# Kernel tuning notes

Hardware: AMD Instinct MI355X
Metric: run time of the kernel (lower is better)

## Reference

```python
import jax, jax.numpy as jnp
import numpy as np

B, S, D = 2, 1024, 4096          # batch, prefill seqlen, model dim
H, KVH, HD = 32, 8, 128          # q heads, kv heads, head dim
MAX = 2048                       # kv-cache capacity
THETA = 1000000.0
REP = H // KVH


def _rope_tables(pos):
    # pos: [S] int -> cos/sin [S, HD]
    inv_freq = 1.0 / (THETA ** (jnp.arange(0, HD, 2, dtype=jnp.float32) / HD))
    freqs = pos[:, None].astype(jnp.float32) * inv_freq[None, :]
    emb = jnp.concatenate([freqs, freqs], axis=-1)
    return jnp.cos(emb), jnp.sin(emb)


def _rotate_half(t):
    t1, t2 = jnp.split(t, 2, axis=-1)
    return jnp.concatenate([-t2, t1], axis=-1)


def setup_inputs() -> dict:
    key = jax.random.key(0)
    k = jax.random.split(key, 8)
    sc = 1.0 / np.sqrt(D)
    x = jax.random.normal(k[0], (B, S, D), jnp.float32)
    storage_idx = jnp.arange(S, dtype=jnp.int32)
    cache = jnp.zeros((2, 1, B, KVH, MAX, HD), jnp.float32)
    causal = jnp.tril(jnp.ones((MAX, MAX), bool))
    mask = jnp.where(causal, 0.0, -1e9).astype(jnp.float32)
    Wq = jax.random.normal(k[1], (D, H * HD), jnp.float32) * sc
    bq = jax.random.normal(k[2], (H * HD,), jnp.float32) * 0.01
    Wk = jax.random.normal(k[3], (D, KVH * HD), jnp.float32) * sc
    bk = jax.random.normal(k[4], (KVH * HD,), jnp.float32) * 0.01
    Wv = jax.random.normal(k[5], (D, KVH * HD), jnp.float32) * sc
    bv = jax.random.normal(k[6], (KVH * HD,), jnp.float32) * 0.01
    Wo = jax.random.normal(k[7], (H * HD, D), jnp.float32) * sc
    return {"x": x, "storage_idx": storage_idx, "cache": cache, "mask": mask,
            "Wq": Wq, "bq": bq, "Wk": Wk, "bk": bk, "Wv": Wv, "bv": bv, "Wo": Wo}


def reference(x, storage_idx, cache, mask, Wq, bq, Wk, bk, Wv, bv, Wo):
    bsz, seqlen, _ = x.shape
    # QKV projections -> [b, heads, s, hd]
    xq = (x @ Wq + bq).reshape(bsz, seqlen, H, HD).transpose(0, 2, 1, 3)
    xk = (x @ Wk + bk).reshape(bsz, seqlen, KVH, HD).transpose(0, 2, 1, 3)
    xv = (x @ Wv + bv).reshape(bsz, seqlen, KVH, HD).transpose(0, 2, 1, 3)
    # inline RoPE at positions storage_idx
    cos, sin = _rope_tables(storage_idx)       # [s, hd]
    cos = cos[None, None]                      # [1,1,s,hd]
    sin = sin[None, None]
    xq = xq * cos + _rotate_half(xq) * sin
    xk = xk * cos + _rotate_half(xk) * sin
    # KV-cache scatter (index_copy_ on dim -2 at storage_idx)
    keys = cache[0, 0].at[:, :, storage_idx, :].set(xk)    # [b, kvh, MAX, hd]
    values = cache[1, 0].at[:, :, storage_idx, :].set(xv)
    # GQA: repeat kv heads
    keys = jnp.repeat(keys, REP, axis=1)       # [b, H, MAX, hd]
    values = jnp.repeat(values, REP, axis=1)
    # attention with additive mask rows gathered at storage_idx
    scores = jnp.einsum('bhqd,bhkd->bhqk', xq, keys) / np.sqrt(HD)
    scores = scores + mask[storage_idx][None, None]        # [b, H, s, MAX]
    attn = jax.nn.softmax(scores, axis=-1)
    out = jnp.einsum('bhqk,bhkd->bhqd', attn, values)
    out = out.transpose(0, 2, 1, 3).reshape(bsz, seqlen, H * HD)
    return out @ Wo
```

## Files before the change

### kernel.cpp

```cpp
#include <hip/hip_runtime.h>
#include <hip/hip_bf16.h>

typedef unsigned short u16;
typedef unsigned int   u32;
using bf16x8 = __attribute__((ext_vector_type(8))) short;
using f32x4  = __attribute__((ext_vector_type(4))) float;

#define AS1 __attribute__((address_space(1)))
#define AS3 __attribute__((address_space(3)))

static constexpr int S_   = 1024;
static constexpr int D_   = 4096;
static constexpr int H_   = 32;
static constexpr int KVH_ = 8;
static constexpr int HD_  = 128;
static constexpr int NQKV = H_*HD_ + 2*KVH_*HD_;

__device__ __forceinline__ u16 f2bf(float f) {
  union { float f; u32 u; } v; v.f = f;
  u32 r = v.u + 0x7FFFu + ((v.u >> 16) & 1u);
  return (u16)(r >> 16);
}

__global__ void k_convert(const float* __restrict__ src, u16* __restrict__ dst, int n4) {
  int i = blockIdx.x * blockDim.x + threadIdx.x;
  if (i >= n4) return;
  float4 v = ((const float4*)src)[i];
  ushort4 o;
  o.x = f2bf(v.x); o.y = f2bf(v.y); o.z = f2bf(v.z); o.w = f2bf(v.w);
  ((ushort4*)dst)[i] = o;
}

__global__ void k_transpose_w(const float* __restrict__ src, u16* __restrict__ dst,
                              int K, int N) {
  __shared__ float t[32][33];
  int k0 = blockIdx.y * 32, n0 = blockIdx.x * 32;
  int tx = threadIdx.x, ty = threadIdx.y;
#pragma unroll
  for (int i = 0; i < 4; ++i)
    t[ty + i*8][tx] = src[(size_t)(k0 + ty + i*8) * N + n0 + tx];
  __syncthreads();
#pragma unroll
  for (int i = 0; i < 4; ++i)
    dst[(size_t)(n0 + ty + i*8) * K + k0 + tx] = f2bf(t[tx][ty + i*8]);
}

__global__ void k_transpose_v(const u16* __restrict__ src, u16* __restrict__ dst) {
  __shared__ u16 t[32][33];
  int bg = blockIdx.z;
  int s0 = blockIdx.x * 32, h0 = blockIdx.y * 32;
  src += (size_t)bg * S_ * HD_;
  dst += (size_t)bg * S_ * HD_;
  int tx = threadIdx.x, ty = threadIdx.y;
#pragma unroll
  for (int i = 0; i < 4; ++i)
    t[ty + i*8][tx] = src[(size_t)(s0 + ty + i*8) * HD_ + h0 + tx];
  __syncthreads();
#pragma unroll
  for (int i = 0; i < 4; ++i)
    dst[(size_t)(h0 + ty + i*8) * S_ + s0 + tx] = t[tx][ty + i*8];
}

__global__ void k_rope(const int* __restrict__ sidx, float* __restrict__ cosd,
                       float* __restrict__ sind) {
  int i = blockIdx.x * blockDim.x + threadIdx.x;
  int s = i >> 6, d = i & 63;
  float pos  = (float)sidx[s];
  float invf = expf(-0.21586735246819178f * (float)d);
  float ph   = pos * invf;
  cosd[i] = cosf(ph);
  sind[i] = sinf(ph);
}

template<int BN>
__global__ __launch_bounds__(512, 2) void k_gemm3(
    const u16* __restrict__ A, const u16* __restrict__ Bt,
    float* __restrict__ C, int N, int K)
{
  constexpr int WN = BN/4, NJ = WN/16, NH = NJ/2;
  constexpr int ABYT = 256*128, BBYT = BN*128, STEP = ABYT+BBYT;
  __shared__ __align__(16) char lds[2*STEP];

  const int cpx = (int)gridDim.x >> 3;
  const int wkid = ((int)blockIdx.x & 7)*cpx + ((int)blockIdx.x >> 3);
  const int NT = N / BN;
  const int m0 = (wkid / NT) * 256, n0 = (wkid % NT) * BN;
  const int tid = threadIdx.x, w = tid>>6, lane = tid&63;
  const int l15 = lane&15, l4 = lane>>4;
  const int wr = w>>2, wc = w&3;
  const int row0 = tid>>3;
  const int ss = (tid&7) ^ (row0&7);
  const int NK = K >> 6;

  f32x4 acc[8][NJ];
#pragma unroll
  for (int i = 0; i < 8; ++i)
#pragma unroll
    for (int j = 0; j < NJ; ++j) acc[i][j] = (f32x4){0.f,0.f,0.f,0.f};

  bf16x8 af[4][2];
  bf16x8 bf[2][NH][2];

#define CHUNK(kt_, part_, r0c_)                                               \
  __builtin_amdgcn_global_load_lds(                                           \
    (AS1 void*)(((part_) ? Bt + (size_t)(n0 + (r0c_) + row0)*K                \
                         : A  + (size_t)(m0 + (r0c_) + row0)*K)               \
                + (size_t)(kt_)*64 + ss*8),                                   \
    (AS3 void*)(lds + ((kt_)&1)*STEP + (part_)*ABYT + (r0c_)*128 + w*1024),   \
    16, 0, 0)

#define LOAD_A(mh_)                                                           \
  _Pragma("unroll") for (int i = 0; i < 4; ++i)                               \
  _Pragma("unroll") for (int kk = 0; kk < 2; ++kk) {                          \
    int row = wr*128 + (mh_)*64 + i*16 + l15;                                 \
    af[i][kk] = *(const bf16x8*)(lA + row*128 + (((kk*4+l4) ^ (row&7)) << 4)); }

#define LOAD_B(nh_)                                                           \
  _Pragma("unroll") for (int jj = 0; jj < NH; ++jj)                           \
  _Pragma("unroll") for (int kk = 0; kk < 2; ++kk) {                          \
    int row = wc*WN + ((nh_)*NH + jj)*16 + l15;                               \
    bf[nh_][jj][kk] = *(const bf16x8*)(lB + row*128 + (((kk*4+l4) ^ (row&7)) << 4)); }

#define MFMA_PH(mh_, nh_)                                                     \
  __builtin_amdgcn_s_setprio(1);                                              \
  _Pragma("unroll") for (int i = 0; i < 4; ++i)                               \
  _Pragma("unroll") for (int jj = 0; jj < NH; ++jj)                           \
  _Pragma("unroll") for (int kk = 0; kk < 2; ++kk)                            \
    acc[(mh_)*4+i][(nh_)*NH+jj] = __builtin_amdgcn_mfma_f32_16x16x32_bf16(    \
        af[i][kk], bf[nh_][jj][kk], acc[(mh_)*4+i][(nh_)*NH+jj], 0, 0, 0);    \
  __builtin_amdgcn_s_setprio(0);

#define BAR   __builtin_amdgcn_s_barrier()
#define SCHB  __builtin_amdgcn_sched_barrier(0)
#define WLGKM asm volatile("s_waitcnt lgkmcnt(0)" ::: "memory")

  CHUNK(0,0,0); CHUNK(0,0,64); CHUNK(0,0,128); CHUNK(0,0,192);
  CHUNK(0,1,0); CHUNK(0,1,64);
  if constexpr (BN == 256) { CHUNK(0,1,128); CHUNK(0,1,192); }
  CHUNK(1,0,0); CHUNK(1,0,128);
  asm volatile("s_waitcnt vmcnt(2)" ::: "memory");
  BAR; SCHB;

  for (int kt = 0; kt < NK; ++kt) {
    const char* lA = lds + (kt&1)*STEP;
    const char* lB = lA + ABYT;
    LOAD_A(0); LOAD_B(0);
    if (kt+1 < NK) { CHUNK(kt+1,0,64); CHUNK(kt+1,0,192); }
    BAR; WLGKM; SCHB;
    MFMA_PH(0,0);
    BAR;
    LOAD_B(1);
    if (kt+1 < NK) {
      CHUNK(kt+1,1,0); CHUNK(kt+1,1,64);
      if constexpr (BN == 256) { CHUNK(kt+1,1,128); CHUNK(kt+1,1,192); }
    }
    BAR; WLGKM; SCHB;
    MFMA_PH(0,1);
    BAR;
    LOAD_A(1);
    if (kt+2 < NK) { CHUNK(kt+2,0,0); CHUNK(kt+2,0,128); }
    BAR; WLGKM; SCHB;
    MFMA_PH(1,0);
    BAR;
    if (kt+2 < NK) asm volatile("s_waitcnt vmcnt(2)" ::: "memory");
    else           asm volatile("s_waitcnt vmcnt(0)" ::: "memory");
    BAR; WLGKM; SCHB;
    MFMA_PH(1,1);
    BAR;
  }
#undef CHUNK
#undef LOAD_A
#undef LOAD_B
#undef MFMA_PH

#pragma unroll
  for (int i = 0; i < 8; ++i)
#pragma unroll
    for (int j = 0; j < NJ; ++j) {
      int r0 = m0 + wr*128 + i*16 + l4*4;
      int c0 = n0 + wc*WN + j*16 + l15;
#pragma unroll
      for (int r = 0; r < 4; ++r)
        C[(size_t)(r0 + r) * N + c0] = acc[i][j][r];
    }
}

__global__ void k_pack(const float* __restrict__ Cq,
                       const float* __restrict__ bq, const float* __restrict__ bk,
                       const float* __restrict__ bv,
                       const float* __restrict__ cosd, const float* __restrict__ sind,
                       u16* __restrict__ qb, u16* __restrict__ kb, u16* __restrict__ vb) {
  int t = blockIdx.x;
  int b = t >> 10, s = t & 1023;
  const float* row = Cq + (size_t)t * NQKV;
  const float* cs = cosd + s*64;
  const float* sn = sind + s*64;
  const float qscale = 0.08838834764831845f;
  for (int c = threadIdx.x; c < H_*HD_; c += blockDim.x) {
    int h = c >> 7, d = c & 127;
    float v = row[c] + bq[c];
    float o;
    if (d < 64) { float p = row[c + 64] + bq[c + 64]; o = v*cs[d]    - p*sn[d]; }
    else        { float p = row[c - 64] + bq[c - 64]; o = v*cs[d-64] + p*sn[d-64]; }
    qb[(((size_t)b*H_ + h)*S_ + s)*HD_ + d] = f2bf(o * qscale);
  }
  for (int c = threadIdx.x; c < KVH_*HD_; c += blockDim.x) {
    int g = c >> 7, d = c & 127;
    float v = row[H_*HD_ + c] + bk[c];
    float o;
    if (d < 64) { float p = row[H_*HD_ + c + 64] + bk[c + 64]; o = v*cs[d]    - p*sn[d]; }
    else        { float p = row[H_*HD_ + c - 64] + bk[c - 64]; o = v*cs[d-64] + p*sn[d-64]; }
    size_t idx = (((size_t)b*KVH_ + g)*S_ + s)*HD_ + d;
    kb[idx] = f2bf(o);
    vb[idx] = f2bf(row[H_*HD_ + KVH_*HD_ + c] + bv[c]);
  }
}

__global__ __launch_bounds__(256, 4) void k_attn(
    const u16* __restrict__ Q, const u16* __restrict__ Kc,
    const u16* __restrict__ Vt, u16* __restrict__ AO)
{
  __shared__ __align__(16) char Kls[2][16384];
  __shared__ __align__(16) char Vls[2][16384];
  __shared__ u16 Pl[4][1024];

  int id = blockIdx.x;
  int slot = id >> 3;
  int bg   = (id & 7)*2 + (slot & 1);
  int rem  = slot >> 1;
  int h_in = rem & 3, bx = rem >> 2;
  int b = bg >> 3, g = bg & 7, h = g*4 + h_in;
  int tA = bx, tB = 15 - bx;

  int tid = threadIdx.x, w = tid >> 6, lane = tid & 63;
  int l15 = lane & 15, l4 = lane >> 4;
  const u16* Qh = Q  + ((size_t)b*H_   + h) * S_ * HD_;
  const u16* Kp = Kc + ((size_t)b*KVH_ + g) * S_ * HD_;
  const u16* Vp = Vt + ((size_t)b*KVH_ + g) * (size_t)HD_ * S_;
  u16* AOh = AO + ((size_t)b*S_) * (H_*HD_) + h*HD_;
  char* Pw = (char*)&Pl[w][0];

  int kOff[4], vOff[4];
#pragma unroll
  for (int c = 0; c < 4; ++c) {
    int ci = c*256 + tid;
    int krow = ci >> 4, ks = ci & 15;
    kOff[c] = krow * HD_ + ((ks & 8) | ((ks & 7) ^ (krow & 7))) * 8;
    int vrow = ci >> 3, vs = ci & 7;
    vOff[c] = vrow * S_ + (vs ^ (vrow & 7)) * 8;
  }

#define ASTAGE(kv_, bb_) {                                                    \
    const u16* ks_ = Kp + (size_t)(kv_) * 64 * HD_;                           \
    const u16* vs_ = Vp + (size_t)(kv_) * 64;                                 \
    _Pragma("unroll") for (int c = 0; c < 4; ++c) {                           \
      __builtin_amdgcn_global_load_lds((AS1 void*)(ks_ + kOff[c]),            \
          (AS3 void*)(&Kls[bb_][0] + c*4096 + w*1024), 16, 0, 0);             \
      __builtin_amdgcn_global_load_lds((AS1 void*)(vs_ + vOff[c]),            \
          (AS3 void*)(&Vls[bb_][0] + c*4096 + w*1024), 16, 0, 0); } }

  bf16x8 qf[4];
#pragma unroll
  for (int kc = 0; kc < 4; ++kc)
    qf[kc] = *(const bf16x8*)(Qh + (size_t)(tA*64 + w*16 + l15)*HD_ + kc*32 + l4*8);

  f32x4 o[8];
#pragma unroll
  for (int n = 0; n < 8; ++n) o[n] = (f32x4){0.f,0.f,0.f,0.f};
  float mrow[4] = {-3e38f,-3e38f,-3e38f,-3e38f};
  float lrow[4] = {0.f,0.f,0.f,0.f};

  ASTAGE(0, 0);
  asm volatile("s_waitcnt vmcnt(0)" ::: "memory");
  __builtin_amdgcn_s_barrier();

  const int NIT = tA + tB + 2;
  int buf = 0;
  for (int it = 0; it < NIT; ++it) {
    bool phA = (it <= tA);
    int kv = phA ? it : it - tA - 1;
    int qt = phA ? tA : tB;
    if (it + 1 < NIT) {
      int kvn = (it + 1 <= tA) ? it + 1 : it - tA;
      ASTAGE(kvn, buf ^ 1);
    }
    const char* Ksb = &Kls[buf][0];
    const char* Vsb = &Vls[buf][0];

    f32x4 sc[4];
    __builtin_amdgcn_s_setprio(1);
#pragma unroll
    for (int ct = 0; ct < 4; ++ct) {
      f32x4 s4 = (f32x4){0.f,0.f,0.f,0.f};
#pragma unroll
      for (int kc = 0; kc < 4; ++kc) {
        int row = ct*16 + l15, s = kc*4 + l4;
        bf16x8 kf = *(const bf16x8*)(Ksb + row*256 + ((((s & 7) ^ (row & 7)) | (s & 8)) << 4));
        s4 = __builtin_amdgcn_mfma_f32_16x16x32_bf16(qf[kc], kf, s4, 0, 0, 0);
      }
      sc[ct] = s4;
    }
    __builtin_amdgcn_s_setprio(0);

    if (kv == qt) {
      int qrow0 = qt*64 + w*16;
#pragma unroll
      for (int ct = 0; ct < 4; ++ct)
#pragma unroll
        for (int r = 0; r < 4; ++r) {
          int col = kv*64 + ct*16 + l15;
          if (col > qrow0 + l4*4 + r) sc[ct][r] = -1e9f;
        }
    }

    float f[4];
#pragma unroll
    for (int r = 0; r < 4; ++r) {
      float mx = fmaxf(fmaxf(sc[0][r], sc[1][r]), fmaxf(sc[2][r], sc[3][r]));
      mx = fmaxf(mx, __shfl_xor(mx, 1));
      mx = fmaxf(mx, __shfl_xor(mx, 2));
      mx = fmaxf(mx, __shfl_xor(mx, 4));
      mx = fmaxf(mx, __shfl_xor(mx, 8));
      float nm = fmaxf(mrow[r], mx);
      f[r] = __expf(mrow[r] - nm);
      mrow[r] = nm;
    }
    float rs[4] = {0.f,0.f,0.f,0.f};
#pragma unroll
    for (int ct = 0; ct < 4; ++ct)
#pragma unroll
      for (int r = 0; r < 4; ++r) {
        float p = __expf(sc[ct][r] - mrow[r]);
        rs[r] += p;
        int row = l4*4 + r, col = ct*16 + l15;
        int byte = row*128 + (((col >> 3) ^ (row & 7)) << 4) + (col & 7)*2;
        *(u16*)(Pw + byte) = f2bf(p);
      }
#pragma unroll
    for (int r = 0; r < 4; ++r) {
      float sum = rs[r];
      sum += __shfl_xor(sum, 1);
      sum += __shfl_xor(sum, 2);
      sum += __shfl_xor(sum, 4);
      sum += __shfl_xor(sum, 8);
      lrow[r] = lrow[r]*f[r] + sum;
    }
#pragma unroll
    for (int n = 0; n < 8; ++n)
#pragma unroll
      for (int r = 0; r < 4; ++r) o[n][r] *= f[r];

    __builtin_amdgcn_s_setprio(1);
#pragma unroll
    for (int kk = 0; kk < 2; ++kk) {
      int pbyte = l15*128 + (((kk*4 + l4) ^ (l15 & 7)) << 4);
      bf16x8 pf = *(const bf16x8*)(Pw + pbyte);
#pragma unroll
      for (int n = 0; n < 8; ++n) {
        int vrow = n*16 + l15, s = kk*4 + l4;
        bf16x8 vf = *(const bf16x8*)(Vsb + vrow*128 + ((s ^ (vrow & 7)) << 4));
        o[n] = __builtin_amdgcn_mfma_f32_16x16x32_bf16(pf, vf, o[n], 0, 0, 0);
      }
    }
    __builtin_amdgcn_s_setprio(0);

    if (it == tA) {
#pragma unroll
      for (int n = 0; n < 8; ++n)
#pragma unroll
        for (int r = 0; r < 4; ++r) {
          int srow = tA*64 + w*16 + l4*4 + r;
          AOh[(size_t)srow * (H_*HD_) + n*16 + l15] = f2bf(o[n][r] / lrow[r]);
        }
#pragma unroll
      for (int n = 0; n < 8; ++n) o[n] = (f32x4){0.f,0.f,0.f,0.f};
#pragma unroll
      for (int r = 0; r < 4; ++r) { mrow[r] = -3e38f; lrow[r] = 0.f; }
#pragma unroll
      for (int kc = 0; kc < 4; ++kc)
        qf[kc] = *(const bf16x8*)(Qh + (size_t)(tB*64 + w*16 + l15)*HD_ + kc*32 + l4*8);
    }

    asm volatile("s_waitcnt vmcnt(0)" ::: "memory");
    __builtin_amdgcn_s_barrier();
    buf ^= 1;
  }
#undef ASTAGE

#pragma unroll
  for (int n = 0; n < 8; ++n)
#pragma unroll
    for (int r = 0; r < 4; ++r) {
      int srow = tB*64 + w*16 + l4*4 + r;
      AOh[(size_t)srow * (H_*HD_) + n*16 + l15] = f2bf(o[n][r] / lrow[r]);
    }
}

extern "C" void kernel_launch(void* const* d_in, const int* in_sizes, int n_in,
                              void* d_out, int out_size, void* d_ws, size_t ws_size,
                              hipStream_t stream) {
  (void)in_sizes; (void)n_in; (void)out_size; (void)ws_size;
  const float* x   = (const float*)d_in[0];
  const int*   sid = (const int*)  d_in[1];
  const float* Wq  = (const float*)d_in[4];
  const float* bq  = (const float*)d_in[5];
  const float* Wk  = (const float*)d_in[6];
  const float* bk  = (const float*)d_in[7];
  const float* Wv  = (const float*)d_in[8];
  const float* bv  = (const float*)d_in[9];
  const float* Wo  = (const float*)d_in[10];
  float* out = (float*)d_out;

  char* ws = (char*)d_ws;
  u16*   xb   = (u16*)  (ws);
  u16*   WB   = (u16*)  (ws + 16777216);
  u16*   WoT  = (u16*)  (ws + 67108864);
  float* Cq   = (float*)(ws + 100663296);
  u16*   qb   = (u16*)  (ws + 150994944);
  u16*   kb   = (u16*)  (ws + 167772160);
  u16*   vb   = (u16*)  (ws + 171966464);
  u16*   VT   = (u16*)  (ws + 176160768);
  float* cosd = (float*)(ws + 180355072);
  float* sind = (float*)(ws + 180617216);
  u16*   AO   = xb;

  dim3 tb(32, 8);
  k_convert<<<8192, 256, 0, stream>>>(x, xb, (2048*4096)/4);
  k_transpose_w<<<dim3(128,128), tb, 0, stream>>>(Wq, WB, 4096, 4096);
  k_transpose_w<<<dim3( 32,128), tb, 0, stream>>>(Wk, WB + (size_t)4096*4096, 4096, 1024);
  k_transpose_w<<<dim3( 32,128), tb, 0, stream>>>(Wv, WB + (size_t)5120*4096, 4096, 1024);
  k_transpose_w<<<dim3(128,128), tb, 0, stream>>>(Wo, WoT, 4096, 4096);
  k_rope<<<256, 256, 0, stream>>>(sid, cosd, sind);
  k_gemm3<256><<<192, 512, 0, stream>>>(xb, WB, Cq, NQKV, 4096);
  k_pack<<<2048, 256, 0, stream>>>(Cq, bq, bk, bv, cosd, sind, qb, kb, vb);
  k_transpose_v<<<dim3(32,4,16), tb, 0, stream>>>(vb, VT);
  k_attn<<<512, 256, 0, stream>>>(qb, kb, VT, AO);
  k_gemm3<128><<<256, 512, 0, stream>>>(AO, WoT, out, 4096, 4096);
}
```

Baseline: 339.4 us.

## Fuse bias, RoPE and bf16 packing into QKV GEMM epilogue

Measured after the change: 315.0 us. -7.2%, faster.

```diff
diff --git a/kernel.cpp b/kernel.cpp
--- a/kernel.cpp
+++ b/kernel.cpp
@@ -70,6 +70,145 @@
   float ph   = pos * invf;
   cosd[i] = cosf(ph);
   sind[i] = sinf(ph);
+}
+
+__global__ __launch_bounds__(512, 2) void k_gemmq(
+    const u16* __restrict__ A, const u16* __restrict__ Bt,
+    const float* __restrict__ bq, const float* __restrict__ bk,
+    const float* __restrict__ bv,
+    const float* __restrict__ cosd, const float* __restrict__ sind,
+    u16* __restrict__ qb, u16* __restrict__ kb, u16* __restrict__ vb)
+{
+  constexpr int K = 4096;
+  constexpr int ABYT = 256*128, BBYT = 256*128, STEP = ABYT+BBYT;
+  __shared__ __align__(16) char lds[2*STEP];
+
+  const int cpx = (int)gridDim.x >> 3;
+  const int wkid = ((int)blockIdx.x & 7)*cpx + ((int)blockIdx.x >> 3);
+  const int NT = 24;
+  const int m0 = (wkid / NT) * 256, n0 = (wkid % NT) * 256;
+  const int tid = threadIdx.x, w = tid>>6, lane = tid&63;
+  const int l15 = lane&15, l4 = lane>>4;
+  const int wr = w>>1, wc = w&1;
+  const int row0 = tid>>3;
+  const int ss = (tid&7) ^ (row0&7);
+  const int NK = K >> 6;
+
+  f32x4 acc[4][8];
+#pragma unroll
+  for (int i = 0; i < 4; ++i)
+#pragma unroll
+    for (int j = 0; j < 8; ++j) acc[i][j] = (f32x4){0.f,0.f,0.f,0.f};
+
+  bf16x8 af[2][2];
+  bf16x8 bfr[2][4][2];
+
+#define QCHUNK(kt_, part_, r0c_)                                              \
+  __builtin_amdgcn_global_load_lds(                                           \
+    (AS1 void*)(((part_) ? Bt + (size_t)(n0 + (r0c_) + row0)*K                \
+                         : A  + (size_t)(m0 + (r0c_) + row0)*K)               \
+                + (size_t)(kt_)*64 + ss*8),                                   \
+    (AS3 void*)(lds + ((kt_)&1)*STEP + (part_)*ABYT + (r0c_)*128 + w*1024),   \
+    16, 0, 0)
+
+#define QLOAD_A(mh_)                                                          \
+  _Pragma("unroll") for (int i2 = 0; i2 < 2; ++i2)                            \
+  _Pragma("unroll") for (int kk = 0; kk < 2; ++kk) {                          \
+    int row = wr*64 + ((mh_)*2 + i2)*16 + l15;                                \
+    af[i2][kk] = *(const bf16x8*)(lA + row*128 + (((kk*4+l4) ^ (row&7)) << 4)); }
+
+#define QLOAD_B(nh_)                                                          \
+  _Pragma("unroll") for (int jj = 0; jj < 4; ++jj)                            \
+  _Pragma("unroll") for (int kk = 0; kk < 2; ++kk) {                          \
+    int row = wc*128 + ((nh_)*4 + jj)*16 + l15;                               \
+    bfr[nh_][jj][kk] = *(const bf16x8*)(lB + row*128 + (((kk*4+l4) ^ (row&7)) << 4)); }
+
+#define QMFMA(mh_, nh_)                                                       \
+  __builtin_amdgcn_s_setprio(1);                                              \
+  _Pragma("unroll") for (int i2 = 0; i2 < 2; ++i2)                            \
+  _Pragma("unroll") for (int jj = 0; jj < 4; ++jj)                            \
+  _Pragma("unroll") for (int kk = 0; kk < 2; ++kk)                            \
+    acc[(mh_)*2+i2][(nh_)*4+jj] = __builtin_amdgcn_mfma_f32_16x16x32_bf16(    \
+        af[i2][kk], bfr[nh_][jj][kk], acc[(mh_)*2+i2][(nh_)*4+jj], 0, 0, 0);  \
+  __builtin_amdgcn_s_setprio(0);
+
+#define BAR   __builtin_amdgcn_s_barrier()
+#define SCHB  __builtin_amdgcn_sched_barrier(0)
+#define WLGKM asm volatile("s_waitcnt lgkmcnt(0)" ::: "memory")
+
+  QCHUNK(0,0,0); QCHUNK(0,0,64); QCHUNK(0,0,128); QCHUNK(0,0,192);
+  QCHUNK(0,1,0); QCHUNK(0,1,64); QCHUNK(0,1,128); QCHUNK(0,1,192);
+  QCHUNK(1,0,0); QCHUNK(1,0,64); QCHUNK(1,0,128); QCHUNK(1,0,192);
+  QCHUNK(1,1,0); QCHUNK(1,1,64); QCHUNK(1,1,128); QCHUNK(1,1,192);
+  asm volatile("s_waitcnt vmcnt(8)" ::: "memory");
+  BAR; SCHB;
+
+  for (int kt = 0; kt < NK; ++kt) {
+    const char* lA = lds + (kt&1)*STEP;
+    const char* lB = lA + ABYT;
+    QLOAD_A(0); QLOAD_B(0);
+    BAR; WLGKM; SCHB;
+    QMFMA(0,0);
+    BAR;
+    QLOAD_B(1);
+    BAR; WLGKM; SCHB;
+    QMFMA(0,1);
+    BAR;
+    QLOAD_A(1);
+    if (kt+2 < NK) { QCHUNK(kt+2,1,0); QCHUNK(kt+2,1,64); QCHUNK(kt+2,1,128); QCHUNK(kt+2,1,192); }
+    BAR; WLGKM; SCHB;
+    QMFMA(1,0);
+    BAR;
+    if (kt+2 < NK) {
+      QCHUNK(kt+2,0,0); QCHUNK(kt+2,0,64); QCHUNK(kt+2,0,128); QCHUNK(kt+2,0,192);
+      asm volatile("s_waitcnt vmcnt(8)" ::: "memory");
+    } else {
+      asm volatile("s_waitcnt vmcnt(0)" ::: "memory");
+    }
+    BAR; WLGKM; SCHB;
+    QMFMA(1,1);
+    BAR;
+  }
+#undef QCHUNK
+#undef QLOAD_A
+#undef QLOAD_B
+#undef QMFMA
+
+  const int btype = (n0 >= H_*HD_) + (n0 >= H_*HD_ + KVH_*HD_);
+  const int colbase = n0 + wc*128 - (btype==1 ? H_*HD_ : btype==2 ? H_*HD_+KVH_*HD_ : 0);
+  const int hloc = colbase >> 7;
+  const float* bias = btype==0 ? bq : btype==1 ? bk : bv;
+  u16* dst = btype==0 ? qb : btype==1 ? kb : vb;
+  const int nheads = btype==0 ? H_ : KVH_;
+  const float scale = btype==0 ? 0.08838834764831845f : 1.0f;
+
+  float bb[8];
+#pragma unroll
+  for (int j = 0; j < 8; ++j) bb[j] = bias[colbase + j*16 + l15];
+
+#pragma unroll
+  for (int i = 0; i < 4; ++i)
+#pragma unroll
+    for (int r = 0; r < 4; ++r) {
+      int sr = m0 + wr*64 + i*16 + l4*4 + r;
+      int b_ = sr >> 10, s_ = sr & 1023;
+      size_t obase = (((size_t)b_*nheads + hloc)*S_ + s_)*(size_t)HD_;
+      if (btype < 2) {
+#pragma unroll
+        for (int j = 0; j < 4; ++j) {
+          float cs = cosd[s_*64 + j*16 + l15];
+          float sn = sind[s_*64 + j*16 + l15];
+          float lo = acc[i][j][r]   + bb[j];
+          float hi = acc[i][j+4][r] + bb[j+4];
+          dst[obase + j*16 + l15]      = f2bf((lo*cs - hi*sn) * scale);
+          dst[obase + 64 + j*16 + l15] = f2bf((hi*cs + lo*sn) * scale);
+        }
+      } else {
+#pragma unroll
+        for (int j = 0; j < 8; ++j)
+          dst[obase + j*16 + l15] = f2bf(acc[i][j][r] + bb[j]);
+      }
+    }
 }
 
 template<int BN>
@@ -130,10 +269,6 @@
         af[i][kk], bf[nh_][jj][kk], acc[(mh_)*4+i][(nh_)*NH+jj], 0, 0, 0);    \
   __builtin_amdgcn_s_setprio(0);
 
-#define BAR   __builtin_amdgcn_s_barrier()
-#define SCHB  __builtin_amdgcn_sched_barrier(0)
-#define WLGKM asm volatile("s_waitcnt lgkmcnt(0)" ::: "memory")
-
   CHUNK(0,0,0); CHUNK(0,0,64); CHUNK(0,0,128); CHUNK(0,0,192);
   CHUNK(0,1,0); CHUNK(0,1,64);
   if constexpr (BN == 256) { CHUNK(0,1,128); CHUNK(0,1,192); }
@@ -185,40 +320,9 @@
     }
 }
 
-__global__ void k_pack(const float* __restrict__ Cq,
-                       const float* __restrict__ bq, const float* __restrict__ bk,
-                       const float* __restrict__ bv,
-                       const float* __restrict__ cosd, const float* __restrict__ sind,
-                       u16* __restrict__ qb, u16* __restrict__ kb, u16* __restrict__ vb) {
-  int t = blockIdx.x;
-  int b = t >> 10, s = t & 1023;
-  const float* row = Cq + (size_t)t * NQKV;
-  const float* cs = cosd + s*64;
-  const float* sn = sind + s*64;
-  const float qscale = 0.08838834764831845f;
-  for (int c = threadIdx.x; c < H_*HD_; c += blockDim.x) {
-    int h = c >> 7, d = c & 127;
-    float v = row[c] + bq[c];
-    float o;
-    if (d < 64) { float p = row[c + 64] + bq[c + 64]; o = v*cs[d]    - p*sn[d]; }
-    else        { float p = row[c - 64] + bq[c - 64]; o = v*cs[d-64] + p*sn[d-64]; }
-    qb[(((size_t)b*H_ + h)*S_ + s)*HD_ + d] = f2bf(o * qscale);
-  }
-  for (int c = threadIdx.x; c < KVH_*HD_; c += blockDim.x) {
-    int g = c >> 7, d = c & 127;
-    float v = row[H_*HD_ + c] + bk[c];
-    float o;
-    if (d < 64) { float p = row[H_*HD_ + c + 64] + bk[c + 64]; o = v*cs[d]    - p*sn[d]; }
-    else        { float p = row[H_*HD_ + c - 64] + bk[c - 64]; o = v*cs[d-64] + p*sn[d-64]; }
-    size_t idx = (((size_t)b*KVH_ + g)*S_ + s)*HD_ + d;
-    kb[idx] = f2bf(o);
-    vb[idx] = f2bf(row[H_*HD_ + KVH_*HD_ + c] + bv[c]);
-  }
-}
-
 __global__ __launch_bounds__(256, 4) void k_attn(
     const u16* __restrict__ Q, const u16* __restrict__ Kc,
-    const u16* __restrict__ Vt, u16* __restrict__ AO)
+    const u16* __restrict__ Vt, const u16* __restrict__ AOdummy, u16* __restrict__ AO)
 {
   __shared__ __align__(16) char Kls[2][16384];
   __shared__ __align__(16) char Vls[2][16384];
@@ -415,7 +519,6 @@
   u16*   xb   = (u16*)  (ws);
   u16*   WB   = (u16*)  (ws + 16777216);
   u16*   WoT  = (u16*)  (ws + 67108864);
-  float* Cq   = (float*)(ws + 100663296);
   u16*   qb   = (u16*)  (ws + 150994944);
   u16*   kb   = (u16*)  (ws + 167772160);
   u16*   vb   = (u16*)  (ws + 171966464);
@@ -431,9 +534,8 @@
   k_transpose_w<<<dim3( 32,128), tb, 0, stream>>>(Wv, WB + (size_t)5120*4096, 4096, 1024);
   k_transpose_w<<<dim3(128,128), tb, 0, stream>>>(Wo, WoT, 4096, 4096);
   k_rope<<<256, 256, 0, stream>>>(sid, cosd, sind);
-  k_gemm3<256><<<192, 512, 0, stream>>>(xb, WB, Cq, NQKV, 4096);
-  k_pack<<<2048, 256, 0, stream>>>(Cq, bq, bk, bv, cosd, sind, qb, kb, vb);
+  k_gemmq<<<192, 512, 0, stream>>>(xb, WB, bq, bk, bv, cosd, sind, qb, kb, vb);
   k_transpose_v<<<dim3(32,4,16), tb, 0, stream>>>(vb, VT);
-  k_attn<<<512, 256, 0, stream>>>(qb, kb, VT, AO);
+  k_attn<<<512, 256, 0, stream>>>(qb, kb, VT, qb, AO);
   k_gemm3<128><<<256, 512, 0, stream>>>(AO, WoT, out, 4096, 4096);
 }
```
